# Performance work log

Measured on AMD Instinct MI355X. Metric: run time of the kernel, lower is better.

The kernel has to match this reference:

```python
import jax, jax.numpy as jnp
import numpy as np

NOISE_EPS = 1e-2


def setup_inputs() -> dict:
    key = jax.random.key(0)
    ks = jax.random.split(key, 6)
    N, D, E, H = 16384, 512, 8, 1024
    x = jax.random.normal(ks[0], (N, D), jnp.float32)
    eps = jax.random.normal(ks[1], (N, E), jnp.float32)
    w_gate = jax.random.normal(ks[2], (D, E), jnp.float32) * 0.02
    w_noise = jax.random.normal(ks[3], (D, E), jnp.float32) * 0.02
    W_h = jnp.eye(E, dtype=jnp.float32)  # module initializes W_h = eye(num_experts)
    W1 = jax.random.normal(ks[4], (E, D, H), jnp.float32) * 0.02
    b1 = jnp.zeros((E, H), jnp.float32)
    W2 = jax.random.normal(ks[5], (E, H, D), jnp.float32) * 0.02
    b2 = jnp.zeros((E, D), jnp.float32)
    return dict(x=x, eps=eps, w_gate=w_gate, w_noise=w_noise, W_h=W_h,
                W1=W1, b1=b1, W2=W2, b2=b2, k=2, capacity=5120)


def reference(x, eps, w_gate, w_noise, W_h, W1, b1, W2, b2, k, capacity):
    N, D = x.shape
    E = w_gate.shape[1]
    # --- noisy top-k gating ---
    clean_logits = (x @ w_gate) @ W_h                       # [N, E]
    noise_stddev = jax.nn.softplus(x @ w_noise) + NOISE_EPS  # [N, E]
    noisy_logits = clean_logits + eps * noise_stddev
    top_vals, top_idx = jax.lax.top_k(noisy_logits, k)       # [N, k]
    top_gates = jax.nn.softmax(top_vals, axis=-1)
    gates = jnp.zeros((N, E), x.dtype).at[jnp.arange(N)[:, None], top_idx].set(top_gates)
    # --- capacity masking: keep the first `capacity` routed tokens per expert (batch order) ---
    active = gates > 0
    rank = jnp.cumsum(active, axis=0) - 1                    # per-expert arrival rank
    keep = active & (rank < capacity)
    gates = jnp.where(keep, gates, jnp.zeros((), x.dtype))
    # --- dispatch into fixed [E, capacity] buffers (dummy slot absorbs dropped writes) ---
    flat = jnp.where(keep, jnp.arange(E)[None, :] * capacity + rank, E * capacity)  # [N, E]
    tok = jnp.broadcast_to(jnp.arange(N, dtype=jnp.int32)[:, None], (N, E))
    buf = jnp.zeros(E * capacity + 1, jnp.int32).at[flat].set(tok)[:E * capacity].reshape(E, capacity)
    gbuf = jnp.zeros(E * capacity + 1, x.dtype).at[flat].set(gates)[:E * capacity].reshape(E, capacity)
    x_exp = x[buf]                                           # [E, C, D] gather
    # --- per-expert 1-layer FFN (grouped GEMM) ---
    h = jax.nn.relu(jnp.einsum('ecd,edh->ech', x_exp, W1) + b1[:, None, :])
    y_exp = jnp.einsum('ech,eho->eco', h, W2) + b2[:, None, :]
    # --- weighted scatter-combine (unfilled slots have gate 0, so they add nothing) ---
    weighted = y_exp * gbuf[..., None]
    combined = jnp.zeros((N, D), x.dtype).at[buf.reshape(-1)].add(weighted.reshape(-1, D))
    return combined
```

## Files before the change

kernel.cpp:

```cpp
#include <hip/hip_runtime.h>
#include <hip/hip_bf16.h>
#include <cstdint>

#define NTOK 16384
#define DIM 512
#define NEXP 8
#define HID 1024
#define CAPACITY 5120

typedef __attribute__((ext_vector_type(8))) short bf16x8;
typedef __attribute__((ext_vector_type(4))) float f32x4;
typedef unsigned long long u64;

__device__ __forceinline__ unsigned short f2bf(float f) {
    unsigned u = __float_as_uint(f);
    unsigned r = (u + 0x7FFFu + ((u >> 16) & 1u)) >> 16;
    return (unsigned short)r;
}

#define GLDS16(gp, lp) __builtin_amdgcn_global_load_lds( \
    (const __attribute__((address_space(1))) void*)(gp), \
    (__attribute__((address_space(3))) void*)(lp), 16, 0, 0)

__global__ __launch_bounds__(256) void gating_kernel(
    const float* __restrict__ x, const float* __restrict__ eps,
    const float* __restrict__ wg, const float* __restrict__ wn,
    const float* __restrict__ Wh, int2* __restrict__ rec)
{
    int w = threadIdx.x >> 6, lane = threadIdx.x & 63;
    int n = blockIdx.x * 4 + w;
    float ag[8], an[8];
#pragma unroll
    for (int e = 0; e < 8; ++e) { ag[e] = 0.f; an[e] = 0.f; }
    const float* xr = x + (size_t)n * DIM;
#pragma unroll
    for (int i = 0; i < DIM / 64; ++i) {
        int d = i * 64 + lane;
        float xv = xr[d];
        const float4* g4 = reinterpret_cast<const float4*>(wg + (size_t)d * 8);
        const float4* n4 = reinterpret_cast<const float4*>(wn + (size_t)d * 8);
        float4 a0 = g4[0], a1 = g4[1], b0 = n4[0], b1v = n4[1];
        ag[0] += xv * a0.x; ag[1] += xv * a0.y; ag[2] += xv * a0.z; ag[3] += xv * a0.w;
        ag[4] += xv * a1.x; ag[5] += xv * a1.y; ag[6] += xv * a1.z; ag[7] += xv * a1.w;
        an[0] += xv * b0.x; an[1] += xv * b0.y; an[2] += xv * b0.z; an[3] += xv * b0.w;
        an[4] += xv * b1v.x; an[5] += xv * b1v.y; an[6] += xv * b1v.z; an[7] += xv * b1v.w;
    }
#pragma unroll
    for (int off = 32; off; off >>= 1) {
#pragma unroll
        for (int e = 0; e < 8; ++e) {
            ag[e] += __shfl_xor(ag[e], off);
            an[e] += __shfl_xor(an[e], off);
        }
    }
    float noisy[8];
#pragma unroll
    for (int e = 0; e < 8; ++e) {
        float c = 0.f;
#pragma unroll
        for (int j = 0; j < 8; ++j) c += ag[j] * Wh[j * 8 + e];
        float v = an[e];
        float sp = fmaxf(v, 0.f) + log1pf(expf(-fabsf(v)));
        noisy[e] = c + eps[(size_t)n * 8 + e] * (sp + 1e-2f);
    }
    int i1 = 0; float v1 = noisy[0];
#pragma unroll
    for (int e = 1; e < 8; ++e) if (noisy[e] > v1) { v1 = noisy[e]; i1 = e; }
    int i2 = -1; float v2 = -3.4e38f;
#pragma unroll
    for (int e = 0; e < 8; ++e) if (e != i1 && noisy[e] > v2) { v2 = noisy[e]; i2 = e; }
    float ex = expf(v2 - v1);
    float g1 = 1.f / (1.f + ex);
    if (lane == 0)
        rec[n] = make_int2(i1 | (i2 << 8), __float_as_int(g1));
}

__global__ __launch_bounds__(1024) void scan_local(
    const int2* __restrict__ rec, unsigned* __restrict__ lrank, int* __restrict__ btot)
{
    __shared__ u64 wtot[16];
    __shared__ int wprefix[16][8];
    int tid = threadIdx.x, w = tid >> 6, lane = tid & 63;
    int n = blockIdx.x * 1024 + tid;
    int2 r = rec[n];
    int e1 = r.x & 0xFF, e2 = (r.x >> 8) & 0xFF;
    u64 m = (1ULL << (e1 * 8)) | (1ULL << (e2 * 8));
    u64 incl = m;
#pragma unroll
    for (int off = 1; off < 64; off <<= 1) {
        u64 v = __shfl_up(incl, off);
        if (lane >= off) incl += v;
    }
    if (lane == 63) wtot[w] = incl;
    __syncthreads();
    if (tid < 128) {
        int e = tid & 7, ww = tid >> 3;
        int s = 0;
        for (int j = 0; j < ww; ++j) s += (int)((wtot[j] >> (e * 8)) & 0xFF);
        wprefix[ww][e] = s;
        if (ww == 15)
            btot[blockIdx.x * 8 + e] = s + (int)((wtot[15] >> (e * 8)) & 0xFF);
    }
    __syncthreads();
    u64 excl = incl - m;
    unsigned l1 = (unsigned)(wprefix[w][e1] + (int)((excl >> (e1 * 8)) & 0xFF));
    unsigned l2 = (unsigned)(wprefix[w][e2] + (int)((excl >> (e2 * 8)) & 0xFF));
    lrank[n] = l1 | (l2 << 16);
}

__global__ __launch_bounds__(64) void scan_offs(
    const int* __restrict__ btot, int* __restrict__ off, int* __restrict__ counts,
    const int* __restrict__ cap_p)
{
    int e = threadIdx.x;
    if (e >= 8) return;
    int cap = *cap_p; if (cap > CAPACITY) cap = CAPACITY;
    int run = 0;
    for (int b = 0; b < 16; ++b) {
        off[b * 8 + e] = run;
        run += btot[b * 8 + e];
    }
    counts[e] = min(run, cap);
}

__global__ __launch_bounds__(1024) void scatter_k(
    const int2* __restrict__ rec, const unsigned* __restrict__ lrank,
    const int* __restrict__ off, const int* __restrict__ cap_p,
    int* __restrict__ buf, float* __restrict__ gbuf)
{
    int tid = threadIdx.x, b = blockIdx.x;
    int n = b * 1024 + tid;
    int cap = *cap_p; if (cap > CAPACITY) cap = CAPACITY;
    int2 r = rec[n];
    int e1 = r.x & 0xFF, e2 = (r.x >> 8) & 0xFF;
    float g1 = __int_as_float(r.y), g2 = 1.f - g1;
    unsigned lr = lrank[n];
    int r1 = off[b * 8 + e1] + (int)(lr & 0xFFFF);
    int r2 = off[b * 8 + e2] + (int)(lr >> 16);
    if (r1 < cap) { buf[e1 * CAPACITY + r1] = n; gbuf[e1 * CAPACITY + r1] = g1; }
    if (r2 < cap) { buf[e2 * CAPACITY + r2] = n; gbuf[e2 * CAPACITY + r2] = g2; }
}

__global__ __launch_bounds__(256) void cvt_x(const float* __restrict__ in,
                                             unsigned short* __restrict__ out, int n)
{
    int i = (blockIdx.x * 256 + threadIdx.x) * 8;
    if (i >= n) return;
    float4 a = *reinterpret_cast<const float4*>(in + i);
    float4 b = *reinterpret_cast<const float4*>(in + i + 4);
    int4 v;
    v.x = f2bf(a.x) | ((int)f2bf(a.y) << 16);
    v.y = f2bf(a.z) | ((int)f2bf(a.w) << 16);
    v.z = f2bf(b.x) | ((int)f2bf(b.y) << 16);
    v.w = f2bf(b.z) | ((int)f2bf(b.w) << 16);
    *reinterpret_cast<int4*>(out + i) = v;
}

__global__ __launch_bounds__(256) void tcvt(const float* __restrict__ in,
                                            unsigned short* __restrict__ out, int R, int C)
{
    __shared__ float tile[32][33];
    int z = blockIdx.z;
    int c0 = blockIdx.x * 32, r0 = blockIdx.y * 32;
    int tx = threadIdx.x, ty = threadIdx.y;
    const float* inz = in + (size_t)z * R * C;
    unsigned short* outz = out + (size_t)z * R * C;
#pragma unroll
    for (int j = 0; j < 32; j += 8)
        tile[ty + j][tx] = inz[(size_t)(r0 + ty + j) * C + c0 + tx];
    __syncthreads();
#pragma unroll
    for (int j = 0; j < 32; j += 8)
        outz[(size_t)(c0 + ty + j) * R + r0 + tx] = f2bf(tile[tx][ty + j]);
}

template <int MODE>
__global__ __launch_bounds__(256, 4) void ffn_gemm(
    const unsigned short* __restrict__ A, const unsigned short* __restrict__ Bt,
    const float* __restrict__ bias, unsigned short* __restrict__ Hout,
    float* __restrict__ Out, const int* __restrict__ buf,
    const float* __restrict__ gbuf, const int* __restrict__ counts,
    int Ka, int Nd)
{
    int flat = blockIdx.x + gridDim.x * (blockIdx.y + gridDim.y * blockIdx.z);
    int e  = flat & 7;
    int rr = flat >> 3;
    int q8 = rr % 8;
    int tm = rr / 8;
    int tn, kh;
    if (MODE == 0) { tn = q8 >> 1; kh = q8 & 1; }
    else           { tn = q8;      kh = 0; }

    int cnt = counts[e];
    if (tm * 128 >= cnt) return;
    int tid = threadIdx.x, w = tid >> 6, lane = tid & 63;
    int q = lane >> 4, rl = lane & 15;
    int ebase = e * CAPACITY;

    __shared__ __align__(16) char lds[32768];
    char* As = lds;
    char* Bs = lds + 16384;

    unsigned aoff[4], boff[4];
#pragma unroll
    for (int i = 0; i < 4; ++i) {
        int p = (w * 4 + i) * 64 + lane;
        int row = p >> 3, kp = p & 7;
        int c = kp ^ (row & 7);
        int slot = tm * 128 + row;
        if (MODE == 1) {
            int tok = (slot < cnt) ? buf[ebase + slot] : 0;
            aoff[i] = (unsigned)tok * Ka + c * 8;
        } else {
            aoff[i] = (unsigned)(ebase + slot) * Ka + c * 8;
        }
        boff[i] = (unsigned)(e * Nd + tn * 128 + row) * Ka + c * 8;
    }

    f32x4 acc[4][4];
#pragma unroll
    for (int mi = 0; mi < 4; ++mi)
#pragma unroll
        for (int ni = 0; ni < 4; ++ni)
            acc[mi][ni] = (f32x4){0.f, 0.f, 0.f, 0.f};

    int wm = w >> 1, wn = w & 1;
    int kbeg = (MODE == 0) ? kh * (Ka >> 1) : 0;
    int kend = kbeg + ((MODE == 0) ? (Ka >> 1) : Ka);

    for (int k0 = kbeg; k0 < kend; k0 += 64) {
#pragma unroll
        for (int i = 0; i < 4; ++i) {
            GLDS16(A + aoff[i] + k0, As + (w * 4 + i) * 1024);
            GLDS16(Bt + boff[i] + k0, Bs + (w * 4 + i) * 1024);
        }
        __syncthreads();
#pragma unroll
        for (int kk = 0; kk < 2; ++kk) {
            bf16x8 af[4], bfr[4];
#pragma unroll
            for (int mi = 0; mi < 4; ++mi) {
                int row = wm * 64 + mi * 16 + rl;
                int cc = (kk * 4 + q) ^ (row & 7);
                af[mi] = *reinterpret_cast<const bf16x8*>(As + row * 128 + cc * 16);
            }
#pragma unroll
            for (int ni = 0; ni < 4; ++ni) {
                int row = wn * 64 + ni * 16 + rl;
                int cc = (kk * 4 + q) ^ (row & 7);
                bfr[ni] = *reinterpret_cast<const bf16x8*>(Bs + row * 128 + cc * 16);
            }
#pragma unroll
            for (int mi = 0; mi < 4; ++mi)
#pragma unroll
                for (int ni = 0; ni < 4; ++ni)
                    acc[mi][ni] = __builtin_amdgcn_mfma_f32_16x16x32_bf16(
                        af[mi], bfr[ni], acc[mi][ni], 0, 0, 0);
        }
        __syncthreads();
    }

    if (MODE == 1) {
#pragma unroll
        for (int ni = 0; ni < 4; ++ni) {
            int gcol = tn * 128 + wn * 64 + ni * 16 + rl;
            float bv = bias[e * Nd + gcol];
#pragma unroll
            for (int mi = 0; mi < 4; ++mi) {
#pragma unroll
                for (int r = 0; r < 4; ++r) {
                    int grow = tm * 128 + wm * 64 + mi * 16 + q * 4 + r;
                    float v = fmaxf(acc[mi][ni][r] + bv, 0.f);
                    Hout[(size_t)(ebase + grow) * HID + gcol] = f2bf(v);
                }
            }
        }
    } else {
#pragma unroll
        for (int ni = 0; ni < 4; ++ni) {
            int gcol = tn * 128 + wn * 64 + ni * 16 + rl;
            float bv = kh ? 0.f : bias[e * Nd + gcol];
#pragma unroll
            for (int mi = 0; mi < 4; ++mi) {
#pragma unroll
                for (int r = 0; r < 4; ++r) {
                    int grow = tm * 128 + wm * 64 + mi * 16 + q * 4 + r;
                    if (grow < cnt) {
                        int tok = buf[ebase + grow];
                        float g = gbuf[ebase + grow];
                        float v = (acc[mi][ni][r] + bv) * g;
                        atomicAdd(Out + (size_t)tok * DIM + gcol, v);
                    }
                }
            }
        }
    }
}

extern "C" void kernel_launch(void* const* d_in, const int* in_sizes, int n_in,
                              void* d_out, int out_size, void* d_ws, size_t ws_size,
                              hipStream_t stream)
{
    const float* x   = (const float*)d_in[0];
    const float* eps = (const float*)d_in[1];
    const float* wg  = (const float*)d_in[2];
    const float* wn  = (const float*)d_in[3];
    const float* Wh  = (const float*)d_in[4];
    const float* W1  = (const float*)d_in[5];
    const float* b1  = (const float*)d_in[6];
    const float* W2  = (const float*)d_in[7];
    const float* b2  = (const float*)d_in[8];
    const int* capp  = (const int*)d_in[10];

    char* ws = (char*)d_ws;
    unsigned short* xg   = (unsigned short*)(ws);
    unsigned short* w1t  = (unsigned short*)(ws + 41943040);
    unsigned short* w2t  = (unsigned short*)(ws + 50331648);
    unsigned short* hK   = (unsigned short*)(ws + 58720256);
    int*      buf    = (int*)     (ws + 142606336);
    float*    gbuf   = (float*)   (ws + 142770176);
    int2*     rec    = (int2*)    (ws + 142934016);
    unsigned* lrank  = (unsigned*)(ws + 143065088);
    int*      btot   = (int*)     (ws + 143130624);
    int*      off    = (int*)     (ws + 143131136);
    int*      counts = (int*)     (ws + 143131648);

    float* out = (float*)d_out;
    hipMemsetAsync(out, 0, (size_t)out_size * sizeof(float), stream);

    gating_kernel<<<NTOK / 4, 256, 0, stream>>>(x, eps, wg, wn, Wh, rec);
    scan_local<<<16, 1024, 0, stream>>>(rec, lrank, btot);
    scan_offs<<<1, 64, 0, stream>>>(btot, off, counts, capp);
    scatter_k<<<16, 1024, 0, stream>>>(rec, lrank, off, capp, buf, gbuf);
    cvt_x<<<NTOK * DIM / 8 / 256, 256, 0, stream>>>(x, xg, NTOK * DIM);
    tcvt<<<dim3(HID / 32, DIM / 32, NEXP), dim3(32, 8), 0, stream>>>(W1, w1t, DIM, HID);
    tcvt<<<dim3(DIM / 32, HID / 32, NEXP), dim3(32, 8), 0, stream>>>(W2, w2t, HID, DIM);

    ffn_gemm<1><<<dim3(CAPACITY / 128, HID / 128, NEXP), 256, 0, stream>>>(
        xg, w1t, b1, hK, nullptr, buf, gbuf, counts, DIM, HID);
    ffn_gemm<0><<<dim3(CAPACITY / 128, 8, NEXP), 256, 0, stream>>>(
        hK, w2t, b2, nullptr, out, buf, gbuf, counts, HID, DIM);
}
```

Measured before the change: 276.5 us.

## Halve GEMM K-tile to 32 and drop split-K in second FFN GEMM

The grouped FFN GEMM now stages a K-slice of 32 instead of 64 per iteration, which halves LDS use to 16 KB and adjusts the XOR swizzle to the narrower rows. The second GEMM no longer splits K into two halves, so each output tile is computed by one block and does half as many atomic adds to the output. The grid for that GEMM shrinks to DIM/128 column tiles. The cost is twice as many barrier-separated iterations with less MFMA work between syncs, and fewer blocks in the second GEMM.

```diff
diff --git a/kernel.cpp b/kernel.cpp
--- a/kernel.cpp
+++ b/kernel.cpp
@@ -185,11 +185,8 @@
     int flat = blockIdx.x + gridDim.x * (blockIdx.y + gridDim.y * blockIdx.z);
     int e  = flat & 7;
     int rr = flat >> 3;
-    int q8 = rr % 8;
-    int tm = rr / 8;
-    int tn, kh;
-    if (MODE == 0) { tn = q8 >> 1; kh = q8 & 1; }
-    else           { tn = q8;      kh = 0; }
+    int tn = rr % gridDim.y;
+    int tm = rr / gridDim.y;
 
     int cnt = counts[e];
     if (tm * 128 >= cnt) return;
@@ -197,16 +194,16 @@
     int q = lane >> 4, rl = lane & 15;
     int ebase = e * CAPACITY;
 
-    __shared__ __align__(16) char lds[32768];
+    __shared__ __align__(16) char lds[16384];
     char* As = lds;
-    char* Bs = lds + 16384;
-
-    unsigned aoff[4], boff[4];
-#pragma unroll
-    for (int i = 0; i < 4; ++i) {
-        int p = (w * 4 + i) * 64 + lane;
-        int row = p >> 3, kp = p & 7;
-        int c = kp ^ (row & 7);
+    char* Bs = lds + 8192;
+
+    unsigned aoff[2], boff[2];
+#pragma unroll
+    for (int i = 0; i < 2; ++i) {
+        int p = (w * 2 + i) * 64 + lane;
+        int row = p >> 2, kp = p & 3;
+        int c = kp ^ ((row >> 1) & 3);
         int slot = tm * 128 + row;
         if (MODE == 1) {
             int tok = (slot < cnt) ? buf[ebase + slot] : 0;
@@ -225,38 +222,31 @@
             acc[mi][ni] = (f32x4){0.f, 0.f, 0.f, 0.f};
 
     int wm = w >> 1, wn = w & 1;
-    int kbeg = (MODE == 0) ? kh * (Ka >> 1) : 0;
-    int kend = kbeg + ((MODE == 0) ? (Ka >> 1) : Ka);
-
-    for (int k0 = kbeg; k0 < kend; k0 += 64) {
-#pragma unroll
-        for (int i = 0; i < 4; ++i) {
-            GLDS16(A + aoff[i] + k0, As + (w * 4 + i) * 1024);
-            GLDS16(Bt + boff[i] + k0, Bs + (w * 4 + i) * 1024);
-        }
+    int ccb = (q ^ ((rl >> 1) & 3)) << 4;
+
+    for (int k0 = 0; k0 < Ka; k0 += 32) {
+        GLDS16(A + aoff[0] + k0, As + (w * 2 + 0) * 1024);
+        GLDS16(A + aoff[1] + k0, As + (w * 2 + 1) * 1024);
+        GLDS16(Bt + boff[0] + k0, Bs + (w * 2 + 0) * 1024);
+        GLDS16(Bt + boff[1] + k0, Bs + (w * 2 + 1) * 1024);
         __syncthreads();
-#pragma unroll
-        for (int kk = 0; kk < 2; ++kk) {
-            bf16x8 af[4], bfr[4];
-#pragma unroll
-            for (int mi = 0; mi < 4; ++mi) {
-                int row = wm * 64 + mi * 16 + rl;
-                int cc = (kk * 4 + q) ^ (row & 7);
-                af[mi] = *reinterpret_cast<const bf16x8*>(As + row * 128 + cc * 16);
-            }
-#pragma unroll
-            for (int ni = 0; ni < 4; ++ni) {
-                int row = wn * 64 + ni * 16 + rl;
-                int cc = (kk * 4 + q) ^ (row & 7);
-                bfr[ni] = *reinterpret_cast<const bf16x8*>(Bs + row * 128 + cc * 16);
-            }
-#pragma unroll
-            for (int mi = 0; mi < 4; ++mi)
-#pragma unroll
-                for (int ni = 0; ni < 4; ++ni)
-                    acc[mi][ni] = __builtin_amdgcn_mfma_f32_16x16x32_bf16(
-                        af[mi], bfr[ni], acc[mi][ni], 0, 0, 0);
-        }
+        bf16x8 af[4], bfr[4];
+#pragma unroll
+        for (int mi = 0; mi < 4; ++mi) {
+            int row = wm * 64 + mi * 16 + rl;
+            af[mi] = *reinterpret_cast<const bf16x8*>(As + row * 64 + ccb);
+        }
+#pragma unroll
+        for (int ni = 0; ni < 4; ++ni) {
+            int row = wn * 64 + ni * 16 + rl;
+            bfr[ni] = *reinterpret_cast<const bf16x8*>(Bs + row * 64 + ccb);
+        }
+#pragma unroll
+        for (int mi = 0; mi < 4; ++mi)
+#pragma unroll
+            for (int ni = 0; ni < 4; ++ni)
+                acc[mi][ni] = __builtin_amdgcn_mfma_f32_16x16x32_bf16(
+                    af[mi], bfr[ni], acc[mi][ni], 0, 0, 0);
         __syncthreads();
     }
 
@@ -279,7 +269,7 @@
 #pragma unroll
         for (int ni = 0; ni < 4; ++ni) {
             int gcol = tn * 128 + wn * 64 + ni * 16 + rl;
-            float bv = kh ? 0.f : bias[e * Nd + gcol];
+            float bv = bias[e * Nd + gcol];
 #pragma unroll
             for (int mi = 0; mi < 4; ++mi) {
 #pragma unroll
@@ -338,6 +328,6 @@
 
     ffn_gemm<1><<<dim3(CAPACITY / 128, HID / 128, NEXP), 256, 0, stream>>>(
         xg, w1t, b1, hK, nullptr, buf, gbuf, counts, DIM, HID);
-    ffn_gemm<0><<<dim3(CAPACITY / 128, 8, NEXP), 256, 0, stream>>>(
+    ffn_gemm<0><<<dim3(CAPACITY / 128, DIM / 128, NEXP), 256, 0, stream>>>(
         hK, w2t, b2, nullptr, out, buf, gbuf, counts, HID, DIM);
 }
```

New measurement: 252.3 us. -8.8%, faster.

## Use 256x128 GEMM tiles with 512-thread blocks and drop split-K in second GEMM

Applied to the files above, without the earlier changes.

Both expert FFN GEMMs now use 256-row by 128-column tiles computed by 8 waves (512 threads), so each B tile loaded into LDS is reused across twice as many rows. The second GEMM no longer splits K in half, which halves the atomic adds into the output and removes the extra bias logic. The cost is fewer, larger blocks, 48KB of LDS per block, and longer per-block K loops, which can reduce occupancy and leave a larger partially idle tail when expert counts are not multiples of 256.

```diff
diff --git a/kernel.cpp b/kernel.cpp
--- a/kernel.cpp
+++ b/kernel.cpp
@@ -175,7 +175,7 @@
 }
 
 template <int MODE>
-__global__ __launch_bounds__(256, 4) void ffn_gemm(
+__global__ __launch_bounds__(512, 4) void ffn_gemm(
     const unsigned short* __restrict__ A, const unsigned short* __restrict__ Bt,
     const float* __restrict__ bias, unsigned short* __restrict__ Hout,
     float* __restrict__ Out, const int* __restrict__ buf,
@@ -185,35 +185,37 @@
     int flat = blockIdx.x + gridDim.x * (blockIdx.y + gridDim.y * blockIdx.z);
     int e  = flat & 7;
     int rr = flat >> 3;
-    int q8 = rr % 8;
-    int tm = rr / 8;
-    int tn, kh;
-    if (MODE == 0) { tn = q8 >> 1; kh = q8 & 1; }
-    else           { tn = q8;      kh = 0; }
+    int tn = rr % gridDim.y;
+    int tm = rr / gridDim.y;
 
     int cnt = counts[e];
-    if (tm * 128 >= cnt) return;
+    if (tm * 256 >= cnt) return;
     int tid = threadIdx.x, w = tid >> 6, lane = tid & 63;
     int q = lane >> 4, rl = lane & 15;
     int ebase = e * CAPACITY;
-
-    __shared__ __align__(16) char lds[32768];
-    char* As = lds;
-    char* Bs = lds + 16384;
-
-    unsigned aoff[4], boff[4];
+    int wm = w >> 1, wn = w & 1;
+
+    __shared__ __align__(16) char lds[49152];
+
+    unsigned aoff[4], boff[2];
 #pragma unroll
     for (int i = 0; i < 4; ++i) {
-        int p = (w * 4 + i) * 64 + lane;
+        int p = i * 512 + tid;
         int row = p >> 3, kp = p & 7;
         int c = kp ^ (row & 7);
-        int slot = tm * 128 + row;
+        int slot = tm * 256 + row;
         if (MODE == 1) {
             int tok = (slot < cnt) ? buf[ebase + slot] : 0;
             aoff[i] = (unsigned)tok * Ka + c * 8;
         } else {
             aoff[i] = (unsigned)(ebase + slot) * Ka + c * 8;
         }
+    }
+#pragma unroll
+    for (int i = 0; i < 2; ++i) {
+        int p = i * 512 + tid;
+        int row = p >> 3, kp = p & 7;
+        int c = kp ^ (row & 7);
         boff[i] = (unsigned)(e * Nd + tn * 128 + row) * Ka + c * 8;
     }
 
@@ -224,16 +226,13 @@
         for (int ni = 0; ni < 4; ++ni)
             acc[mi][ni] = (f32x4){0.f, 0.f, 0.f, 0.f};
 
-    int wm = w >> 1, wn = w & 1;
-    int kbeg = (MODE == 0) ? kh * (Ka >> 1) : 0;
-    int kend = kbeg + ((MODE == 0) ? (Ka >> 1) : Ka);
-
-    for (int k0 = kbeg; k0 < kend; k0 += 64) {
-#pragma unroll
-        for (int i = 0; i < 4; ++i) {
-            GLDS16(A + aoff[i] + k0, As + (w * 4 + i) * 1024);
-            GLDS16(Bt + boff[i] + k0, Bs + (w * 4 + i) * 1024);
-        }
+    for (int k0 = 0; k0 < Ka; k0 += 64) {
+#pragma unroll
+        for (int i = 0; i < 4; ++i)
+            GLDS16(A + aoff[i] + k0, lds + i * 8192 + tid * 16);
+#pragma unroll
+        for (int i = 0; i < 2; ++i)
+            GLDS16(Bt + boff[i] + k0, lds + 32768 + i * 8192 + tid * 16);
         __syncthreads();
 #pragma unroll
         for (int kk = 0; kk < 2; ++kk) {
@@ -242,13 +241,13 @@
             for (int mi = 0; mi < 4; ++mi) {
                 int row = wm * 64 + mi * 16 + rl;
                 int cc = (kk * 4 + q) ^ (row & 7);
-                af[mi] = *reinterpret_cast<const bf16x8*>(As + row * 128 + cc * 16);
+                af[mi] = *reinterpret_cast<const bf16x8*>(lds + row * 128 + cc * 16);
             }
 #pragma unroll
             for (int ni = 0; ni < 4; ++ni) {
                 int row = wn * 64 + ni * 16 + rl;
                 int cc = (kk * 4 + q) ^ (row & 7);
-                bfr[ni] = *reinterpret_cast<const bf16x8*>(Bs + row * 128 + cc * 16);
+                bfr[ni] = *reinterpret_cast<const bf16x8*>(lds + 32768 + row * 128 + cc * 16);
             }
 #pragma unroll
             for (int mi = 0; mi < 4; ++mi)
@@ -269,7 +268,7 @@
             for (int mi = 0; mi < 4; ++mi) {
 #pragma unroll
                 for (int r = 0; r < 4; ++r) {
-                    int grow = tm * 128 + wm * 64 + mi * 16 + q * 4 + r;
+                    int grow = tm * 256 + wm * 64 + mi * 16 + q * 4 + r;
                     float v = fmaxf(acc[mi][ni][r] + bv, 0.f);
                     Hout[(size_t)(ebase + grow) * HID + gcol] = f2bf(v);
                 }
@@ -279,12 +278,12 @@
 #pragma unroll
         for (int ni = 0; ni < 4; ++ni) {
             int gcol = tn * 128 + wn * 64 + ni * 16 + rl;
-            float bv = kh ? 0.f : bias[e * Nd + gcol];
+            float bv = bias[e * Nd + gcol];
 #pragma unroll
             for (int mi = 0; mi < 4; ++mi) {
 #pragma unroll
                 for (int r = 0; r < 4; ++r) {
-                    int grow = tm * 128 + wm * 64 + mi * 16 + q * 4 + r;
+                    int grow = tm * 256 + wm * 64 + mi * 16 + q * 4 + r;
                     if (grow < cnt) {
                         int tok = buf[ebase + grow];
                         float g = gbuf[ebase + grow];
@@ -336,8 +335,8 @@
     tcvt<<<dim3(HID / 32, DIM / 32, NEXP), dim3(32, 8), 0, stream>>>(W1, w1t, DIM, HID);
     tcvt<<<dim3(DIM / 32, HID / 32, NEXP), dim3(32, 8), 0, stream>>>(W2, w2t, HID, DIM);
 
-    ffn_gemm<1><<<dim3(CAPACITY / 128, HID / 128, NEXP), 256, 0, stream>>>(
+    ffn_gemm<1><<<dim3(CAPACITY / 256, HID / 128, NEXP), 512, 0, stream>>>(
         xg, w1t, b1, hK, nullptr, buf, gbuf, counts, DIM, HID);
-    ffn_gemm<0><<<dim3(CAPACITY / 128, 8, NEXP), 256, 0, stream>>>(
+    ffn_gemm<0><<<dim3(CAPACITY / 256, DIM / 128, NEXP), 512, 0, stream>>>(
         hK, w2t, b2, nullptr, out, buf, gbuf, counts, HID, DIM);
 }
```

New measurement: 249.8 us. 9.7% less time.
